# Performance work log

Measured on AMD Instinct MI355X. Metric: run time of the kernel, lower is better.

The kernel has to match this reference:

```python
import jax, jax.numpy as jnp
import numpy as np

NPOINT = 8192
NSAMPLE = 16
SUPPORT_TH = 100.0  # 10 ** 2


def sqdist(a, b):
    # a:[B,N,3], b:[B,M,3] -> squared pairwise distances [B,N,M]
    return (jnp.sum(a * a, -1)[:, :, None] + jnp.sum(b * b, -1)[:, None, :]
            - 2.0 * jnp.einsum('bnc,bmc->bnm', a, b))


def fps_single(xyz, npoint):
    # farthest point sampling; xyz:[N,3] -> [npoint] int32 indices (start at 0)
    N = xyz.shape[0]

    def body(carry, _):
        dist, far = carry
        d = jnp.sum((xyz - xyz[far]) ** 2, -1)
        dist = jnp.minimum(dist, d)
        return (dist, jnp.argmax(dist).astype(jnp.int32)), far

    init = (jnp.full((N,), 1e10, xyz.dtype), jnp.int32(0))
    _, idx = jax.lax.scan(body, init, None, length=npoint)
    return idx


def gather(p, idx):
    # p:[B,N,C], idx:[B,...] -> [B,...,C]
    return jax.vmap(lambda pp, ii: pp[ii])(p, idx)


def instance_norm(x, g, b):
    # InstanceNorm2d(affine=True): normalize over spatial dims (S,K) per (B,C)
    mu = jnp.mean(x, axis=(1, 2), keepdims=True)
    var = jnp.var(x, axis=(1, 2), keepdims=True)
    return (x - mu) / jnp.sqrt(var + 1e-5) * g + b


def set_abstraction(xyz, points, npoint, ws, gs, bs):
    # PointNetSetAbstraction, radius=None -> knn grouping. xyz:[B,3,N], points:[B,C,N]
    xt = xyz.transpose(0, 2, 1)    # [B,N,3]
    pt = points.transpose(0, 2, 1)  # [B,N,C]
    fps_idx = jax.vmap(fps_single, (0, None))(jax.lax.stop_gradient(xt), npoint)  # [B,S]
    new_xyz = gather(xt, fps_idx)                               # [B,S,3]
    d = sqdist(new_xyz, xt)                                     # [B,S,N]
    _, knn_idx = jax.lax.top_k(-d, NSAMPLE)                     # [B,S,K]
    g_xyz = gather(xt, knn_idx) - new_xyz[:, :, None, :]        # [B,S,K,3]
    g_pts = gather(pt, knn_idx)                                 # [B,S,K,C]
    x = jnp.concatenate([g_xyz, g_pts], -1)                     # [B,S,K,3+C]
    for w, g, b in zip(ws, gs, bs):                             # 1x1 conv -> IN -> relu
        x = jax.nn.relu(instance_norm(jnp.einsum('bskc,cd->bskd', x, w), g, b))
    feats = jnp.max(x, axis=2)                                  # max over nsample -> [B,S,D]
    return new_xyz.transpose(0, 2, 1), feats.transpose(0, 2, 1)


def feature_prop(xyz1, xyz2, points2):
    # PointNetFeaturePropogation with mlp=[]: 3-NN inverse-distance interpolation
    # xyz1:[B,3,N], xyz2:[B,3,S], points2:[B,C,S] -> [B,C,N]
    x1 = xyz1.transpose(0, 2, 1)
    x2 = xyz2.transpose(0, 2, 1)
    p2 = points2.transpose(0, 2, 1)
    d = sqdist(x1, x2)                       # [B,N,S]
    neg, idx = jax.lax.top_k(-d, 3)          # 3 smallest distances
    w = 1.0 / (-neg + 1e-8)
    w = w / jnp.sum(w, -1, keepdims=True)    # [B,N,3]
    nb = gather(p2, idx)                     # [B,N,3,C]
    return jnp.sum(nb * w[..., None], axis=2).transpose(0, 2, 1)


def setup_inputs() -> dict:
    key = jax.random.key(0)
    ks = jax.random.split(key, 16)
    B, N0, N1, N2, N3, CF = 8, 8192, 1024, 512, 256, 256

    def w(k, ci, co):
        return (jax.random.normal(k, (ci, co), jnp.float32) / np.sqrt(ci)).astype(jnp.float32)

    inp = {
        'pc1_l0': jax.random.normal(ks[0], (B, 3, N0), jnp.float32),
        'pc1_l1': jax.random.normal(ks[1], (B, 3, N1), jnp.float32),
        'pc1_l2': jax.random.normal(ks[2], (B, 3, N2), jnp.float32),
        'pc1_l3': jax.random.normal(ks[3], (B, 3, N3), jnp.float32),
        'pc2_l3': jax.random.normal(ks[4], (B, 3, N3), jnp.float32),
        'feats1': jax.random.normal(ks[5], (B, CF, N3), jnp.float32),
        'feats2': jax.random.normal(ks[6], (B, CF, N3), jnp.float32),
        'epsilon': jnp.zeros((1,), jnp.float32),
        'sa1_w0': w(ks[7], 6, 32), 'sa1_w1': w(ks[8], 32, 32), 'sa1_w2': w(ks[9], 32, 64),
        'sa1_g0': jnp.ones((32,), jnp.float32), 'sa1_b0': jnp.zeros((32,), jnp.float32),
        'sa1_g1': jnp.ones((32,), jnp.float32), 'sa1_b1': jnp.zeros((32,), jnp.float32),
        'sa1_g2': jnp.ones((64,), jnp.float32), 'sa1_b2': jnp.zeros((64,), jnp.float32),
        'sa2_w0': w(ks[10], 67, 64), 'sa2_w1': w(ks[11], 64, 64), 'sa2_w2': w(ks[12], 64, 128),
        'sa2_g0': jnp.ones((64,), jnp.float32), 'sa2_b0': jnp.zeros((64,), jnp.float32),
        'sa2_g1': jnp.ones((64,), jnp.float32), 'sa2_b1': jnp.zeros((64,), jnp.float32),
        'sa2_g2': jnp.ones((128,), jnp.float32), 'sa2_b2': jnp.zeros((128,), jnp.float32),
    }
    return inp


def reference(pc1_l0, pc1_l1, pc1_l2, pc1_l3, pc2_l3, feats1, feats2, epsilon,
              sa1_w0, sa1_w1, sa1_w2, sa1_g0, sa1_b0, sa1_g1, sa1_b1, sa1_g2, sa1_b2,
              sa2_w0, sa2_w1, sa2_w2, sa2_g0, sa2_b0, sa2_g1, sa2_b1, sa2_g2, sa2_b2):
    eps = jnp.exp(epsilon) + 0.03
    p1 = pc1_l3.transpose(0, 2, 1)   # [B,N3,3]
    p2 = pc2_l3.transpose(0, 2, 1)
    f1 = feats1.transpose(0, 2, 1)   # [B,N3,C]
    f2 = feats2.transpose(0, 2, 1)
    dmat = sqdist(p1, p2)
    support = (dmat < SUPPORT_TH).astype(p1.dtype)
    f1 = f1 / jnp.sqrt(jnp.sum(f1 * f1, -1, keepdims=True) + 1e-8)
    f2 = f2 / jnp.sqrt(jnp.sum(f2 * f2, -1, keepdims=True) + 1e-8)
    C = 1.0 - jnp.einsum('bnc,bmc->bnm', f1, f2)
    corr = jnp.exp(-C / eps) * support
    row = jnp.sum(corr, -1, keepdims=True)
    flow0 = jnp.einsum('bnm,bmc->bnc', corr, p2) / (row + 1e-8) - p1   # [B,N3,3]
    flow0_us = feature_prop(pc1_l2, pc1_l3, flow0.transpose(0, 2, 1))  # [B,3,N2]
    _, cf2 = set_abstraction(pc1_l2, flow0_us, NPOINT // 16,
                             (sa1_w0, sa1_w1, sa1_w2), (sa1_g0, sa1_g1, sa1_g2),
                             (sa1_b0, sa1_b1, sa1_b2))
    cf1 = feature_prop(pc1_l1, pc1_l2, cf2)
    _, cf1 = set_abstraction(pc1_l1, cf1, NPOINT // 8,
                             (sa2_w0, sa2_w1, sa2_w2), (sa2_g0, sa2_g1, sa2_g2),
                             (sa2_b0, sa2_b1, sa2_b2))
    return feature_prop(pc1_l0, pc1_l1, cf1)   # [B,128,N0]
```

## Files before the change

### kernel.cpp

```cpp
#include <hip/hip_runtime.h>
#include <math.h>

#define NB 8
#define N0 8192
#define N1 1024
#define N2 512
#define N3C 256
#define CFEAT 256
#define KNN 16
#define PSTRIDE 256

typedef float v2f __attribute__((ext_vector_type(2)));

static __device__ __forceinline__ v2f pk_add(v2f a, v2f b) {
  v2f r; asm("v_pk_add_f32 %0, %1, %2" : "=v"(r) : "v"(a), "v"(b)); return r;
}
static __device__ __forceinline__ v2f pk_mul(v2f a, v2f b) {
  v2f r; asm("v_pk_mul_f32 %0, %1, %2" : "=v"(r) : "v"(a), "v"(b)); return r;
}

template <int CTRL, int RM>
static __device__ __forceinline__ double dpp_fmax64(double m) {
  int mh = __double2hiint(m), ml = __double2loint(m);
  int ch = __builtin_amdgcn_update_dpp(mh, mh, CTRL, RM, 0xF, false);
  int cl = __builtin_amdgcn_update_dpp(ml, ml, CTRL, RM, 0xF, false);
  return fmax(m, __hiloint2double(ch, cl));
}
static __device__ __forceinline__ double wave_fmax64(double m) {
  m = dpp_fmax64<0x111, 0xF>(m);
  m = dpp_fmax64<0x112, 0xF>(m);
  m = dpp_fmax64<0x114, 0xF>(m);
  m = dpp_fmax64<0x118, 0xF>(m);
  m = dpp_fmax64<0x142, 0xA>(m);
  m = dpp_fmax64<0x143, 0xC>(m);
  return m;
}

template <int CTRL, int RM>
static __device__ __forceinline__ void dpp_minstep(uint32_t& hi, uint32_t& lo) {
  uint32_t chi = (uint32_t)__builtin_amdgcn_update_dpp((int)hi, (int)hi, CTRL, RM, 0xF, false);
  uint32_t clo = (uint32_t)__builtin_amdgcn_update_dpp((int)lo, (int)lo, CTRL, RM, 0xF, false);
  unsigned long long cand = ((unsigned long long)chi << 32) | clo;
  unsigned long long cur  = ((unsigned long long)hi  << 32) | lo;
  if (cand < cur) { hi = chi; lo = clo; }
}
static __device__ __forceinline__ void wave_min_pair(uint32_t& hi, uint32_t& lo) {
  dpp_minstep<0x111, 0xF>(hi, lo);
  dpp_minstep<0x112, 0xF>(hi, lo);
  dpp_minstep<0x114, 0xF>(hi, lo);
  dpp_minstep<0x118, 0xF>(hi, lo);
  dpp_minstep<0x142, 0xA>(hi, lo);
  dpp_minstep<0x143, 0xC>(hi, lo);
}

template <int CTRL, int RM>
static __device__ __forceinline__ float dpp_addstep(float x) {
  int xi = __float_as_int(x);
  int sv = __builtin_amdgcn_update_dpp(xi, xi, CTRL, RM, 0xF, true);
  return x + __int_as_float(sv);
}
static __device__ __forceinline__ float wave_sum63(float x) {
  x = dpp_addstep<0x111, 0xF>(x);
  x = dpp_addstep<0x112, 0xF>(x);
  x = dpp_addstep<0x114, 0xF>(x);
  x = dpp_addstep<0x118, 0xF>(x);
  x = dpp_addstep<0x142, 0xA>(x);
  x = dpp_addstep<0x143, 0xC>(x);
  return x;
}

template <int N>
static __device__ void fps_scan4(const float4* sm, double* kb, int* idx_out) {
  constexpr int PPW = N / 256;
  int tid = threadIdx.x;
  int lane = tid & 63;
  int w = tid >> 6;
  int base = w * (N / 4) + lane * PPW;
  v2f px[PPW / 2], py[PPW / 2], pz[PPW / 2];
  float dist[PPW];
  int nlo[PPW];
#pragma unroll
  for (int k = 0; k < PPW / 2; k++) {
    float4 a = sm[base + 2 * k];
    float4 c = sm[base + 2 * k + 1];
    px[k] = v2f{a.x, c.x}; py[k] = v2f{a.y, c.y}; pz[k] = v2f{a.z, c.z};
    dist[2 * k] = 1e10f; dist[2 * k + 1] = 1e10f;
    nlo[2 * k] = ~(base + 2 * k); nlo[2 * k + 1] = ~(base + 2 * k + 1);
  }
  int far = 0;
  float4 f = sm[0];
  for (int t = 0; t < N; t++) {
    if (tid == 0) idx_out[t] = far;
    v2f vfx = v2f{-f.x, -f.x}, vfy = v2f{-f.y, -f.y}, vfz = v2f{-f.z, -f.z};
#pragma unroll
    for (int k = 0; k < PPW / 2; k++) {
      v2f dx = pk_add(px[k], vfx);
      v2f dy = pk_add(py[k], vfy);
      v2f dz = pk_add(pz[k], vfz);
      v2f dd = pk_add(pk_add(pk_mul(dx, dx), pk_mul(dy, dy)), pk_mul(dz, dz));
      dist[2 * k]     = fminf(dist[2 * k],     dd.x);
      dist[2 * k + 1] = fminf(dist[2 * k + 1], dd.y);
    }
    double tv[PPW / 2];
#pragma unroll
    for (int i = 0; i < PPW / 2; i++)
      tv[i] = fmax(__hiloint2double(__float_as_int(dist[2 * i]),     nlo[2 * i]),
                   __hiloint2double(__float_as_int(dist[2 * i + 1]), nlo[2 * i + 1]));
#pragma unroll
    for (int s = PPW / 4; s >= 1; s >>= 1)
#pragma unroll
      for (int i = 0; i < s; i++) tv[i] = fmax(tv[i], tv[i + s]);
    double m = wave_fmax64(tv[0]);
    if (lane == 63) kb[(t & 1) * 4 + w] = m;
    __syncthreads();
    const double* kq = kb + (t & 1) * 4;
    double M = fmax(fmax(kq[0], kq[1]), fmax(kq[2], kq[3]));
    far = ~__double2loint(M);
    f = sm[far];
  }
}

static __device__ void corr_unit(int u, const float* __restrict__ f1, const float* __restrict__ f2,
                                 const float* __restrict__ p1, const float* __restrict__ p2,
                                 const float* __restrict__ eps_in, float* __restrict__ flow0,
                                 char* smem) {
  float* f1c = (float*)smem;
  float* red = f1c + 256;
  float* p1s = red + 16;
  int b = u / N3C, n = u % N3C;
  int m = threadIdx.x;
  f1c[m] = f1[((size_t)b * CFEAT + m) * N3C + n];
  if (m < 3) p1s[m] = p1[((size_t)b * 3 + m) * N3C + n];
  __syncthreads();
  float eps = expf(eps_in[0]) + 0.03f;
  const float* f2b = f2 + (size_t)b * CFEAT * N3C;
  float dot = 0.f, s1 = 0.f, s2 = 0.f;
  for (int c = 0; c < CFEAT; c++) {
    float a = f1c[c];
    float v = f2b[(size_t)c * N3C + m];
    dot += a * v; s1 += a * a; s2 += v * v;
  }
  float rn1 = 1.0f / sqrtf(s1 + 1e-8f);
  float rn2 = 1.0f / sqrtf(s2 + 1e-8f);
  float Cv = 1.0f - dot * rn1 * rn2;
  float p2x = p2[((size_t)b * 3 + 0) * N3C + m];
  float p2y = p2[((size_t)b * 3 + 1) * N3C + m];
  float p2z = p2[((size_t)b * 3 + 2) * N3C + m];
  float n1v = p1s[0] * p1s[0] + p1s[1] * p1s[1] + p1s[2] * p1s[2];
  float n2v = p2x * p2x + p2y * p2y + p2z * p2z;
  float dd = n1v + n2v - 2.0f * (p1s[0] * p2x + p1s[1] * p2y + p1s[2] * p2z);
  float corr = (dd < 100.0f) ? expf(-Cv / eps) : 0.0f;
  float s0 = corr, t1 = corr * p2x, t2 = corr * p2y, t3 = corr * p2z;
  for (int off = 32; off; off >>= 1) {
    s0 += __shfl_xor(s0, off, 64); t1 += __shfl_xor(t1, off, 64);
    t2 += __shfl_xor(t2, off, 64); t3 += __shfl_xor(t3, off, 64);
  }
  int wid = threadIdx.x >> 6;
  if ((threadIdx.x & 63) == 0) { red[wid] = s0; red[4 + wid] = t1; red[8 + wid] = t2; red[12 + wid] = t3; }
  __syncthreads();
  if (threadIdx.x == 0) {
    float r0 = red[0] + red[1] + red[2] + red[3];
    float r1 = red[4] + red[5] + red[6] + red[7];
    float r2 = red[8] + red[9] + red[10] + red[11];
    float r3 = red[12] + red[13] + red[14] + red[15];
    float inv = 1.0f / (r0 + 1e-8f);
    float* fo = flow0 + ((size_t)b * N3C + n) * 3;
    fo[0] = r1 * inv - p1s[0];
    fo[1] = r2 * inv - p1s[1];
    fo[2] = r3 * inv - p1s[2];
  }
  __syncthreads();
}

__global__ void fps_corr_kernel(const float* __restrict__ xyz_l2, const float* __restrict__ xyz_l1,
                                int* __restrict__ fps1, int* __restrict__ fps2,
                                const float* __restrict__ f1, const float* __restrict__ f2,
                                const float* __restrict__ p1, const float* __restrict__ p2,
                                const float* __restrict__ eps_in, float* __restrict__ flow0) {
  __shared__ __align__(16) char smem[16448];
  int blk = blockIdx.x, tid = threadIdx.x;
  if (blk < 2 * NB) {
    float4* sm = (float4*)smem;
    double* kb = (double*)(smem + 16384);
    if (blk < NB) {
      const float* xb = xyz_l2 + (size_t)blk * 3 * N2;
      for (int i = tid; i < N2; i += 256) {
        float4 v; v.x = xb[i]; v.y = xb[N2 + i]; v.z = xb[2 * N2 + i]; v.w = 0.f;
        sm[i] = v;
      }
      __syncthreads();
      fps_scan4<N2>(sm, kb, fps1 + (size_t)blk * N2);
    } else {
      int b = blk - NB;
      const float* xb = xyz_l1 + (size_t)b * 3 * N1;
      for (int i = tid; i < N1; i += 256) {
        float4 v; v.x = xb[i]; v.y = xb[N1 + i]; v.z = xb[2 * N1 + i]; v.w = 0.f;
        sm[i] = v;
      }
      __syncthreads();
      fps_scan4<N1>(sm, kb, fps2 + (size_t)b * N1);
    }
  } else {
    for (int u = blk - 2 * NB; u < NB * N3C; u += (int)gridDim.x - 2 * NB)
      corr_unit(u, f1, f2, p1, p2, eps_in, flow0, smem);
  }
}

template <int S, int PPL>
static __device__ void knn_impl(const float* __restrict__ xyz, const int* __restrict__ fps_idx,
                                int* __restrict__ knn_out, int gw) {
  int lane = threadIdx.x & 63;
  int b = gw / S, s = gw % S;
  int center = fps_idx[(size_t)b * S + s];
  const float* xb = xyz + (size_t)b * 3 * S;
  float cx = xb[center], cy = xb[S + center], cz = xb[2 * S + center];
  float cn = cx * cx + cy * cy + cz * cz;
  uint32_t kb[PPL];
#pragma unroll
  for (int j = 0; j < PPL; j++) {
    int g = lane * PPL + j;
    float x = xb[g], y = xb[S + g], z = xb[2 * S + g];
    float pn = x * x + y * y + z * z;
    float d = cn + pn - 2.0f * (cx * x + cy * y + cz * z);
    uint32_t bts = __float_as_uint(d);
    kb[j] = bts ^ ((uint32_t)((int)bts >> 31) | 0x80000000u);
  }
  int* ob = knn_out + ((size_t)b * S + s) * KNN;
  for (int r = 0; r < KNN; r++) {
    uint32_t bh = 0xFFFFFFFFu, bl = 0xFFFFFFFFu;
#pragma unroll
    for (int j = 0; j < PPL; j++) {
      unsigned long long cand = ((unsigned long long)kb[j] << 32) | (uint32_t)(lane * PPL + j);
      unsigned long long cur  = ((unsigned long long)bh << 32) | bl;
      if (cand < cur) { bh = kb[j]; bl = (uint32_t)(lane * PPL + j); }
    }
    wave_min_pair(bh, bl);
    uint32_t widx = (uint32_t)__builtin_amdgcn_readlane((int)bl, 63);
    if (lane == 0) ob[r] = (int)widx;
#pragma unroll
    for (int j = 0; j < PPL; j++)
      if ((uint32_t)(lane * PPL + j) == widx) kb[j] = 0xFFFFFFFFu;
  }
}

template <int C, bool TOUT, int S>
static __device__ void fprop_unit(int u, int Npts, const float* __restrict__ xyz1,
                                  const float* __restrict__ xyz2, const float* __restrict__ featT,
                                  float* __restrict__ out, float* smem) {
  float* x2s = smem;
  float* n2s = x2s + 3 * S;
  int tilesPerB = Npts / 256;
  int b = u / tilesPerB;
  int n = (u % tilesPerB) * 256 + threadIdx.x;
  for (int i = threadIdx.x; i < S; i += 256) {
    float xx = xyz2[((size_t)b * 3 + 0) * S + i];
    float yy = xyz2[((size_t)b * 3 + 1) * S + i];
    float zz = xyz2[((size_t)b * 3 + 2) * S + i];
    x2s[i] = xx; x2s[S + i] = yy; x2s[2 * S + i] = zz;
    n2s[i] = xx * xx + yy * yy + zz * zz;
  }
  __syncthreads();
  float X = xyz1[((size_t)b * 3 + 0) * Npts + n];
  float Y = xyz1[((size_t)b * 3 + 1) * Npts + n];
  float Z = xyz1[((size_t)b * 3 + 2) * Npts + n];
  float n1v = X * X + Y * Y + Z * Z;
  float d0 = 1e30f, d1 = 1e30f, d2 = 1e30f;
  int i0 = 0, i1 = 0, i2 = 0;
  for (int s = 0; s < S; s++) {
    float d = n1v + n2s[s] - 2.0f * (X * x2s[s] + Y * x2s[S + s] + Z * x2s[2 * S + s]);
    if (d < d0)      { d2 = d1; i2 = i1; d1 = d0; i1 = i0; d0 = d; i0 = s; }
    else if (d < d1) { d2 = d1; i2 = i1; d1 = d; i1 = s; }
    else if (d < d2) { d2 = d; i2 = s; }
  }
  float w0 = 1.0f / (d0 + 1e-8f), w1 = 1.0f / (d1 + 1e-8f), w2 = 1.0f / (d2 + 1e-8f);
  float wsum = w0 + w1 + w2;
  w0 /= wsum; w1 /= wsum; w2 /= wsum;
  const float* g0 = featT + ((size_t)b * S + i0) * C;
  const float* g1 = featT + ((size_t)b * S + i1) * C;
  const float* g2 = featT + ((size_t)b * S + i2) * C;
  if constexpr (C % 4 == 0) {
    const float4* v0 = (const float4*)g0;
    const float4* v1 = (const float4*)g1;
    const float4* v2 = (const float4*)g2;
#pragma unroll 4
    for (int c4 = 0; c4 < C / 4; c4++) {
      float4 a = v0[c4], bb = v1[c4], cc = v2[c4];
      float4 r;
      r.x = w0 * a.x + w1 * bb.x + w2 * cc.x;
      r.y = w0 * a.y + w1 * bb.y + w2 * cc.y;
      r.z = w0 * a.z + w1 * bb.z + w2 * cc.z;
      r.w = w0 * a.w + w1 * bb.w + w2 * cc.w;
      if constexpr (TOUT) {
        ((float4*)(out + ((size_t)b * Npts + n) * C))[c4] = r;
      } else {
        out[((size_t)b * C + 4 * c4 + 0) * Npts + n] = r.x;
        out[((size_t)b * C + 4 * c4 + 1) * Npts + n] = r.y;
        out[((size_t)b * C + 4 * c4 + 2) * Npts + n] = r.z;
        out[((size_t)b * C + 4 * c4 + 3) * Npts + n] = r.w;
      }
    }
  } else {
#pragma unroll
    for (int c = 0; c < C; c++) {
      float val = w0 * g0[c] + w1 * g1[c] + w2 * g2[c];
      if constexpr (TOUT) out[((size_t)b * Npts + n) * C + c] = val;
      else                out[((size_t)b * C + c) * Npts + n] = val;
    }
  }
}

__global__ void knn_fprop_kernel(const float* __restrict__ xyz_l2, const int* __restrict__ fps1,
                                 int* __restrict__ knn1,
                                 const float* __restrict__ xyz_l1, const int* __restrict__ fps2,
                                 int* __restrict__ knn2,
                                 const float* __restrict__ xyz_l3, const float* __restrict__ flow0,
                                 float* __restrict__ flow0_us) {
  __shared__ float sm[4 * N3C];
  const int KB = (NB * N2 + NB * N1) / 4;
  int blk = blockIdx.x;
  if (blk < KB) {
    int gw = blk * 4 + (threadIdx.x >> 6);
    if (gw < NB * N2) knn_impl<N2, 8>(xyz_l2, fps1, knn1, gw);
    else              knn_impl<N1, 16>(xyz_l1, fps2, knn2, gw - NB * N2);
  } else {
    fprop_unit<3, true, N3C>(blk - KB, N2, xyz_l2, xyz_l3, flow0, flow0_us, sm);
  }
}

template <int C, bool TOUT, int S>
__global__ void fprop_kernel(const float* __restrict__ xyz1, const float* __restrict__ xyz2,
                             const float* __restrict__ featT, float* __restrict__ out, int N) {
  __shared__ float sm[4 * S];
  fprop_unit<C, TOUT, S>(blockIdx.x, N, xyz1, xyz2, featT, out, sm);
}

template <int D>
static __device__ __forceinline__ void write_partials(const float* acc, int b, int bpb,
                                                      float* __restrict__ ps, float* __restrict__ pq) {
  int lane = threadIdx.x & 63;
  int slot = (blockIdx.x - b * bpb) * 4 + (threadIdx.x >> 6);
#pragma unroll
  for (int i = 0; i < D; i++) {
    float s = wave_sum63(acc[i]);
    float q = wave_sum63(acc[i] * acc[i]);
    if (lane == 63) {
      size_t row = (size_t)(b * D + i) * PSTRIDE + slot;
      ps[row] = s; pq[row] = q;
    }
  }
}

template <int CF, int D>
__global__ void mm0p_kernel(const float* __restrict__ xyz, const float* __restrict__ featsT,
                            const int* __restrict__ fps_idx, const int* __restrict__ knn,
                            const float* __restrict__ w, float* __restrict__ y,
                            float* __restrict__ ps, float* __restrict__ pq, int S) {
  const int SK = S * KNN;
  int t = blockIdx.x * 256 + threadIdx.x;
  int b = t / SK, sk = t % SK, s = sk / KNN;
  int nb = knn[(size_t)b * SK + sk];
  int ctr = fps_idx[(size_t)b * S + s];
  const float* xb = xyz + (size_t)b * 3 * S;
  float r0 = xb[nb] - xb[ctr];
  float r1 = xb[S + nb] - xb[S + ctr];
  float r2 = xb[2 * S + nb] - xb[2 * S + ctr];
  float acc[D];
#pragma unroll
  for (int i = 0; i < D; i++)
    acc[i] = fmaf(r0, w[i], fmaf(r1, w[D + i], r2 * w[2 * D + i]));
  const float* pb = featsT + ((size_t)b * S + nb) * CF;
  if constexpr (CF % 4 == 0) {
    const float4* pv = (const float4*)pb;
    for (int c4 = 0; c4 < CF / 4; c4++) {
      float4 v = pv[c4];
      const float* wr = w + (size_t)(3 + 4 * c4) * D;
#pragma unroll
      for (int i = 0; i < D; i++)
        acc[i] = fmaf(v.x, wr[i],
                 fmaf(v.y, wr[D + i],
                 fmaf(v.z, wr[2 * D + i],
                 fmaf(v.w, wr[3 * D + i], acc[i]))));
    }
  } else {
#pragma unroll
    for (int c = 0; c < CF; c++) {
      float xv = pb[c];
      const float* wr = w + (size_t)(3 + c) * D;
#pragma unroll
      for (int i = 0; i < D; i++) acc[i] = fmaf(xv, wr[i], acc[i]);
    }
  }
  float* yb = y + (size_t)b * D * SK + sk;
#pragma unroll
  for (int i = 0; i < D; i++) yb[(size_t)i * SK] = acc[i];
  write_partials<D>(acc, b, SK / 256, ps, pq);
}

template <int Cin, int D>
__global__ void mmnorms_kernel(const float* __restrict__ x, const float* __restrict__ w,
                               const float* __restrict__ ps_in, const float* __restrict__ pq_in,
                               const float* __restrict__ g, const float* __restrict__ beta,
                               float* __restrict__ y, float* __restrict__ ps_out,
                               float* __restrict__ pq_out, int SK) {
  __shared__ float smean[Cin], srstd[Cin];
  const int NS = SK / 64;
  int b = (int)(((size_t)blockIdx.x * 256) / SK);
  {
    const int TPC = 256 / Cin;
    int c = threadIdx.x / TPC, r = threadIdx.x % TPC;
    const float* p1 = ps_in + (size_t)(b * Cin + c) * PSTRIDE;
    const float* p2 = pq_in + (size_t)(b * Cin + c) * PSTRIDE;
    float s = 0.f, q = 0.f;
    for (int j = r; j < NS; j += TPC) { s += p1[j]; q += p2[j]; }
    for (int off = TPC / 2; off; off >>= 1) {
      s += __shfl_down(s, off, 64);
      q += __shfl_down(q, off, 64);
    }
    if (r == 0) {
      float mu = s / (float)SK;
      float var = q / (float)SK - mu * mu;
      smean[c] = mu;
      srstd[c] = 1.0f / sqrtf(var + 1e-5f);
    }
  }
  __syncthreads();
  int t = blockIdx.x * 256 + threadIdx.x;
  int sk = t % SK;
  const float* xb = x + (size_t)b * Cin * SK + sk;
  float* yb = y + (size_t)b * D * SK + sk;
  float acc[D];
#pragma unroll
  for (int i = 0; i < D; i++) acc[i] = 0.f;
  for (int c = 0; c < Cin; c++) {
    float sc = srstd[c] * g[c];
    float sh = fmaf(-smean[c], sc, beta[c]);
    float xv = fmaxf(fmaf(xb[(size_t)c * SK], sc, sh), 0.f);
    const float* wr = w + (size_t)c * D;
#pragma unroll
    for (int i = 0; i < D; i++) acc[i] = fmaf(xv, wr[i], acc[i]);
  }
#pragma unroll
  for (int i = 0; i < D; i++) yb[(size_t)i * SK] = acc[i];
  write_partials<D>(acc, b, SK / 256, ps_out, pq_out);
}

template <int D>
__global__ void maxpool_norms_kernel(const float* __restrict__ y, const float* __restrict__ ps,
                                     const float* __restrict__ pq, const float* __restrict__ g,
                                     const float* __restrict__ beta, float* __restrict__ outT,
                                     int S) {
  __shared__ float sred[8];
  const int SK = S * KNN;
  const int NS = SK / 64;
  int t = blockIdx.x * 256 + threadIdx.x;
  int s = t % S;
  int bd = t / S;
  int d = bd % D, b = bd / D;
  float ssum = 0.f, qsum = 0.f;
  {
    const float* p1 = ps + (size_t)bd * PSTRIDE;
    const float* p2 = pq + (size_t)bd * PSTRIDE;
    for (int j = threadIdx.x; j < NS; j += 256) { ssum += p1[j]; qsum += p2[j]; }
    for (int off = 32; off; off >>= 1) { ssum += __shfl_xor(ssum, off, 64); qsum += __shfl_xor(qsum, off, 64); }
    int wid = threadIdx.x >> 6;
    if ((threadIdx.x & 63) == 0) { sred[wid] = ssum; sred[4 + wid] = qsum; }
    __syncthreads();
    ssum = sred[0] + sred[1] + sred[2] + sred[3];
    qsum = sred[4] + sred[5] + sred[6] + sred[7];
  }
  float mu = ssum / (float)SK;
  float var = qsum / (float)SK - mu * mu;
  float rstd = 1.0f / sqrtf(var + 1e-5f);
  float sc = rstd * g[d];
  float sh = fmaf(-mu, sc, beta[d]);
  const float4* p = (const float4*)(y + (size_t)t * KNN);
  float m = -1e30f;
#pragma unroll
  for (int q = 0; q < 4; q++) {
    float4 v = p[q];
    m = fmaxf(m, fmaf(v.x, sc, sh)); m = fmaxf(m, fmaf(v.y, sc, sh));
    m = fmaxf(m, fmaf(v.z, sc, sh)); m = fmaxf(m, fmaf(v.w, sc, sh));
  }
  outT[((size_t)b * S + s) * D + d] = fmaxf(m, 0.f);
}

extern "C" void kernel_launch(void* const* d_in, const int* in_sizes, int n_in,
                              void* d_out, int out_size, void* d_ws, size_t ws_size,
                              hipStream_t stream) {
  const float* pc1_l0 = (const float*)d_in[0];
  const float* pc1_l1 = (const float*)d_in[1];
  const float* pc1_l2 = (const float*)d_in[2];
  const float* pc1_l3 = (const float*)d_in[3];
  const float* pc2_l3 = (const float*)d_in[4];
  const float* feats1 = (const float*)d_in[5];
  const float* feats2 = (const float*)d_in[6];
  const float* epsilon = (const float*)d_in[7];
  const float* sa1_w[3] = {(const float*)d_in[8], (const float*)d_in[9], (const float*)d_in[10]};
  const float* sa1_g[3] = {(const float*)d_in[11], (const float*)d_in[13], (const float*)d_in[15]};
  const float* sa1_b[3] = {(const float*)d_in[12], (const float*)d_in[14], (const float*)d_in[16]};
  const float* sa2_w[3] = {(const float*)d_in[17], (const float*)d_in[18], (const float*)d_in[19]};
  const float* sa2_g[3] = {(const float*)d_in[20], (const float*)d_in[22], (const float*)d_in[24]};
  const float* sa2_b[3] = {(const float*)d_in[21], (const float*)d_in[23], (const float*)d_in[25]};

  char* ws = (char*)d_ws;
  size_t off = 0;
  auto alloc = [&](size_t bytes) { char* p = ws + off; off += (bytes + 255) & ~(size_t)255; return p; };
  float* bigA     = (float*)alloc((size_t)NB * 128 * N1 * KNN * 4);
  float* bigB     = (float*)alloc((size_t)NB * 64 * N1 * KNN * 4);
  float* psA      = (float*)alloc((size_t)NB * 128 * PSTRIDE * 4);
  float* pqA      = (float*)alloc((size_t)NB * 128 * PSTRIDE * 4);
  float* psB      = (float*)alloc((size_t)NB * 128 * PSTRIDE * 4);
  float* pqB      = (float*)alloc((size_t)NB * 128 * PSTRIDE * 4);
  float* flow0    = (float*)alloc((size_t)NB * N3C * 3 * 4);
  float* flow0_us = (float*)alloc((size_t)NB * N2 * 3 * 4);
  int*   fps1     = (int*)alloc((size_t)NB * N2 * 4);
  int*   knn1     = (int*)alloc((size_t)NB * N2 * KNN * 4);
  float* cf2      = (float*)alloc((size_t)NB * N2 * 64 * 4);
  float* cf1a     = (float*)alloc((size_t)NB * N1 * 64 * 4);
  int*   fps2     = (int*)alloc((size_t)NB * N1 * 4);
  int*   knn2     = (int*)alloc((size_t)NB * N1 * KNN * 4);
  float* cf1b     = (float*)alloc((size_t)NB * N1 * 128 * 4);
  (void)ws_size; (void)in_sizes; (void)n_in; (void)out_size;

  fps_corr_kernel<<<2 * NB + 2048, 256, 0, stream>>>(pc1_l2, pc1_l1, fps1, fps2,
                                                     feats1, feats2, pc1_l3, pc2_l3,
                                                     epsilon, flow0);

  knn_fprop_kernel<<<(NB * N2 + NB * N1) / 4 + NB * (N2 / 256), 256, 0, stream>>>(
      pc1_l2, fps1, knn1, pc1_l1, fps2, knn2, pc1_l3, flow0, flow0_us);

  {
    const int S = N2, SK = S * KNN;
    const int G = NB * SK / 256;
    mm0p_kernel<3, 32><<<G, 256, 0, stream>>>(pc1_l2, flow0_us, fps1, knn1, sa1_w[0],
                                              bigA, psA, pqA, S);
    mmnorms_kernel<32, 32><<<G, 256, 0, stream>>>(bigA, sa1_w[1], psA, pqA, sa1_g[0], sa1_b[0],
                                                  bigB, psB, pqB, SK);
    mmnorms_kernel<32, 64><<<G, 256, 0, stream>>>(bigB, sa1_w[2], psB, pqB, sa1_g[1], sa1_b[1],
                                                  bigA, psA, pqA, SK);
    maxpool_norms_kernel<64><<<NB * 64 * S / 256, 256, 0, stream>>>(bigA, psA, pqA,
                                                                    sa1_g[2], sa1_b[2], cf2, S);
  }

  fprop_kernel<64, true, N2><<<NB * (N1 / 256), 256, 0, stream>>>(pc1_l1, pc1_l2, cf2, cf1a, N1);

  {
    const int S = N1, SK = S * KNN;
    const int G = NB * SK / 256;
    mm0p_kernel<64, 64><<<G, 256, 0, stream>>>(pc1_l1, cf1a, fps2, knn2, sa2_w[0],
                                               bigA, psA, pqA, S);
    mmnorms_kernel<64, 64><<<G, 256, 0, stream>>>(bigA, sa2_w[1], psA, pqA, sa2_g[0], sa2_b[0],
                                                  bigB, psB, pqB, SK);
    mmnorms_kernel<64, 128><<<G, 256, 0, stream>>>(bigB, sa2_w[2], psB, pqB, sa2_g[1], sa2_b[1],
                                                   bigA, psA, pqA, SK);
    maxpool_norms_kernel<128><<<NB * 128 * S / 256, 256, 0, stream>>>(bigA, psA, pqA,
                                                                      sa2_g[2], sa2_b[2], cf1b, S);
  }

  fprop_kernel<128, false, N1><<<NB * (N0 / 256), 256, 0, stream>>>(pc1_l0, pc1_l1, cf1b,
                                                                    (float*)d_out, N0);
}
```

Before: 893.4 us.

## Pass FPS winner coordinates through LDS; split wide 64->128 layer into halves

In the FPS scan, each wave extracts its winning candidate's coordinates with readlane and writes them next to the max key. After the barrier, every thread picks the winning coordinates directly, so the dependent LDS load of sm[far] is removed from the serial per-iteration critical path. Separately, the 64->128 mmnorms layer of the second set abstraction is split into two launches of 64 output channels each, using offset templates. This halves per-thread accumulators, which should lower register pressure, at the cost of reading the input twice and one extra launch.

New measurement: 958.1 us. 1.07x slower.

```diff
diff --git a/kernel.cpp b/kernel.cpp
--- a/kernel.cpp
+++ b/kernel.cpp
@@ -70,8 +70,9 @@
 }
 
 template <int N>
-static __device__ void fps_scan4(const float4* sm, double* kb, int* idx_out) {
+static __device__ void fps_scan4(const float4* sm, double* kbuf, float4* cbuf, int* idx_out) {
   constexpr int PPW = N / 256;
+  constexpr int L2P = (PPW == 2) ? 1 : 2;
   int tid = threadIdx.x;
   int lane = tid & 63;
   int w = tid >> 6;
@@ -88,10 +89,11 @@
     nlo[2 * k] = ~(base + 2 * k); nlo[2 * k + 1] = ~(base + 2 * k + 1);
   }
   int far = 0;
-  float4 f = sm[0];
+  float4 f0 = sm[0];
+  float fx = f0.x, fy = f0.y, fz = f0.z;
   for (int t = 0; t < N; t++) {
     if (tid == 0) idx_out[t] = far;
-    v2f vfx = v2f{-f.x, -f.x}, vfy = v2f{-f.y, -f.y}, vfz = v2f{-f.z, -f.z};
+    v2f vfx = v2f{-fx, -fx}, vfy = v2f{-fy, -fy}, vfz = v2f{-fz, -fz};
 #pragma unroll
     for (int k = 0; k < PPW / 2; k++) {
       v2f dx = pk_add(px[k], vfx);
@@ -110,13 +112,29 @@
     for (int s = PPW / 4; s >= 1; s >>= 1)
 #pragma unroll
       for (int i = 0; i < s; i++) tv[i] = fmax(tv[i], tv[i + s]);
-    double m = wave_fmax64(tv[0]);
-    if (lane == 63) kb[(t & 1) * 4 + w] = m;
+    int myidx = ~__double2loint(tv[0]);
+    float4 cand = sm[myidx];
+    double M = wave_fmax64(tv[0]);
+    int widx = ~__builtin_amdgcn_readlane(__double2loint(M), 63);
+    int wl = (widx - w * (N / 4)) >> L2P;
+    float cx = __int_as_float(__builtin_amdgcn_readlane(__float_as_int(cand.x), wl));
+    float cy = __int_as_float(__builtin_amdgcn_readlane(__float_as_int(cand.y), wl));
+    float cz = __int_as_float(__builtin_amdgcn_readlane(__float_as_int(cand.z), wl));
+    int p = t & 1;
+    if (lane == 63) {
+      kbuf[p * 4 + w] = M;
+      cbuf[p * 4 + w] = make_float4(cx, cy, cz, 0.f);
+    }
     __syncthreads();
-    const double* kq = kb + (t & 1) * 4;
-    double M = fmax(fmax(kq[0], kq[1]), fmax(kq[2], kq[3]));
-    far = ~__double2loint(M);
-    f = sm[far];
+    const double* kq = kbuf + p * 4;
+    const float4* cq = cbuf + p * 4;
+    double k0 = kq[0], k1 = kq[1], k2 = kq[2], k3 = kq[3];
+    float4 c0 = cq[0], c1 = cq[1], c2 = cq[2], c3 = cq[3];
+    double m01 = fmax(k0, k1); float4 s01 = (k1 > k0) ? c1 : c0;
+    double m23 = fmax(k2, k3); float4 s23 = (k3 > k2) ? c3 : c2;
+    double MG  = fmax(m01, m23); float4 cw = (m23 > m01) ? s23 : s01;
+    far = ~__double2loint(MG);
+    fx = cw.x; fy = cw.y; fz = cw.z;
   }
 }
 
@@ -177,11 +195,12 @@
                                 const float* __restrict__ f1, const float* __restrict__ f2,
                                 const float* __restrict__ p1, const float* __restrict__ p2,
                                 const float* __restrict__ eps_in, float* __restrict__ flow0) {
-  __shared__ __align__(16) char smem[16448];
+  __shared__ __align__(16) char smem[16384 + 64 + 128];
   int blk = blockIdx.x, tid = threadIdx.x;
   if (blk < 2 * NB) {
     float4* sm = (float4*)smem;
-    double* kb = (double*)(smem + 16384);
+    double* kbuf = (double*)(smem + 16384);
+    float4* cbuf = (float4*)(smem + 16384 + 64);
     if (blk < NB) {
       const float* xb = xyz_l2 + (size_t)blk * 3 * N2;
       for (int i = tid; i < N2; i += 256) {
@@ -189,7 +208,7 @@
         sm[i] = v;
       }
       __syncthreads();
-      fps_scan4<N2>(sm, kb, fps1 + (size_t)blk * N2);
+      fps_scan4<N2>(sm, kbuf, cbuf, fps1 + (size_t)blk * N2);
     } else {
       int b = blk - NB;
       const float* xb = xyz_l1 + (size_t)b * 3 * N1;
@@ -198,7 +217,7 @@
         sm[i] = v;
       }
       __syncthreads();
-      fps_scan4<N1>(sm, kb, fps2 + (size_t)b * N1);
+      fps_scan4<N1>(sm, kbuf, cbuf, fps2 + (size_t)b * N1);
     }
   } else {
     for (int u = blk - 2 * NB; u < NB * N3C; u += (int)gridDim.x - 2 * NB)
@@ -334,7 +353,7 @@
   fprop_unit<C, TOUT, S>(blockIdx.x, N, xyz1, xyz2, featT, out, sm);
 }
 
-template <int D>
+template <int D, int DTOT, int DOFF>
 static __device__ __forceinline__ void write_partials(const float* acc, int b, int bpb,
                                                       float* __restrict__ ps, float* __restrict__ pq) {
   int lane = threadIdx.x & 63;
@@ -344,7 +363,7 @@
     float s = wave_sum63(acc[i]);
     float q = wave_sum63(acc[i] * acc[i]);
     if (lane == 63) {
-      size_t row = (size_t)(b * D + i) * PSTRIDE + slot;
+      size_t row = (size_t)(b * DTOT + DOFF + i) * PSTRIDE + slot;
       ps[row] = s; pq[row] = q;
     }
   }
@@ -393,10 +412,10 @@
   float* yb = y + (size_t)b * D * SK + sk;
 #pragma unroll
   for (int i = 0; i < D; i++) yb[(size_t)i * SK] = acc[i];
-  write_partials<D>(acc, b, SK / 256, ps, pq);
-}
-
-template <int Cin, int D>
+  write_partials<D, D, 0>(acc, b, SK / 256, ps, pq);
+}
+
+template <int Cin, int D, int DTOT, int DOFF>
 __global__ void mmnorms_kernel(const float* __restrict__ x, const float* __restrict__ w,
                                const float* __restrict__ ps_in, const float* __restrict__ pq_in,
                                const float* __restrict__ g, const float* __restrict__ beta,
@@ -427,7 +446,7 @@
   int t = blockIdx.x * 256 + threadIdx.x;
   int sk = t % SK;
   const float* xb = x + (size_t)b * Cin * SK + sk;
-  float* yb = y + (size_t)b * D * SK + sk;
+  float* yb = y + (size_t)b * DTOT * SK + sk;
   float acc[D];
 #pragma unroll
   for (int i = 0; i < D; i++) acc[i] = 0.f;
@@ -435,13 +454,13 @@
     float sc = srstd[c] * g[c];
     float sh = fmaf(-smean[c], sc, beta[c]);
     float xv = fmaxf(fmaf(xb[(size_t)c * SK], sc, sh), 0.f);
-    const float* wr = w + (size_t)c * D;
+    const float* wr = w + (size_t)c * DTOT + DOFF;
 #pragma unroll
     for (int i = 0; i < D; i++) acc[i] = fmaf(xv, wr[i], acc[i]);
   }
 #pragma unroll
-  for (int i = 0; i < D; i++) yb[(size_t)i * SK] = acc[i];
-  write_partials<D>(acc, b, SK / 256, ps_out, pq_out);
+  for (int i = 0; i < D; i++) yb[(size_t)(DOFF + i) * SK] = acc[i];
+  write_partials<D, DTOT, DOFF>(acc, b, SK / 256, ps_out, pq_out);
 }
 
 template <int D>
@@ -534,10 +553,12 @@
     const int G = NB * SK / 256;
     mm0p_kernel<3, 32><<<G, 256, 0, stream>>>(pc1_l2, flow0_us, fps1, knn1, sa1_w[0],
                                               bigA, psA, pqA, S);
-    mmnorms_kernel<32, 32><<<G, 256, 0, stream>>>(bigA, sa1_w[1], psA, pqA, sa1_g[0], sa1_b[0],
-                                                  bigB, psB, pqB, SK);
-    mmnorms_kernel<32, 64><<<G, 256, 0, stream>>>(bigB, sa1_w[2], psB, pqB, sa1_g[1], sa1_b[1],
-                                                  bigA, psA, pqA, SK);
+    mmnorms_kernel<32, 32, 32, 0><<<G, 256, 0, stream>>>(bigA, sa1_w[1], psA, pqA,
+                                                         sa1_g[0], sa1_b[0],
+                                                         bigB, psB, pqB, SK);
+    mmnorms_kernel<32, 64, 64, 0><<<G, 256, 0, stream>>>(bigB, sa1_w[2], psB, pqB,
+                                                         sa1_g[1], sa1_b[1],
+                                                         bigA, psA, pqA, SK);
     maxpool_norms_kernel<64><<<NB * 64 * S / 256, 256, 0, stream>>>(bigA, psA, pqA,
                                                                     sa1_g[2], sa1_b[2], cf2, S);
   }
@@ -549,10 +570,15 @@
     const int G = NB * SK / 256;
     mm0p_kernel<64, 64><<<G, 256, 0, stream>>>(pc1_l1, cf1a, fps2, knn2, sa2_w[0],
                                                bigA, psA, pqA, S);
-    mmnorms_kernel<64, 64><<<G, 256, 0, stream>>>(bigA, sa2_w[1], psA, pqA, sa2_g[0], sa2_b[0],
-                                                  bigB, psB, pqB, SK);
-    mmnorms_kernel<64, 128><<<G, 256, 0, stream>>>(bigB, sa2_w[2], psB, pqB, sa2_g[1], sa2_b[1],
-                                                   bigA, psA, pqA, SK);
+    mmnorms_kernel<64, 64, 64, 0><<<G, 256, 0, stream>>>(bigA, sa2_w[1], psA, pqA,
+                                                         sa2_g[0], sa2_b[0],
+                                                         bigB, psB, pqB, SK);
+    mmnorms_kernel<64, 64, 128, 0><<<G, 256, 0, stream>>>(bigB, sa2_w[2], psB, pqB,
+                                                          sa2_g[1], sa2_b[1],
+                                                          bigA, psA, pqA, SK);
+    mmnorms_kernel<64, 64, 128, 64><<<G, 256, 0, stream>>>(bigB, sa2_w[2], psB, pqB,
+                                                           sa2_g[1], sa2_b[1],
+                                                           bigA, psA, pqA, SK);
     maxpool_norms_kernel<128><<<NB * 128 * S / 256, 256, 0, stream>>>(bigA, psA, pqA,
                                                                       sa2_g[2], sa2_b[2], cf1b, S);
   }
```
